# Kernel tuning notes

Hardware: AMD Instinct MI355X
Metric: run time of the kernel (lower is better)

## Reference

```python
import jax, jax.numpy as jnp
import numpy as np

DIM = 64; HEADS = 8; WIN = 4; K = 3
B = 8; H = 256; W = 256; WS = H // 2  # 2x2 window grid since ka_win_num=4
L = WIN * K * K            # 36 tokens for kernel self-attention
DH = DIM // HEADS
RED = DIM // 16            # SE reduction (dim>=64 branch)


def setup_inputs() -> dict:
    key = jax.random.key(0)
    ks = jax.random.split(key, 12)
    f = lambda k, s: jax.random.normal(k, s, jnp.float32) * 0.05
    return {
        "x": jax.random.normal(ks[0], (B, DIM, H, W), jnp.float32),
        "conv_w": f(ks[1], (WIN, DIM, DIM, K, K)),   # per-window Conv2d weights
        "w_qkv": f(ks[2], (3 * DIM, DIM)),
        "b_qkv": f(ks[3], (3 * DIM,)),
        "w_out": f(ks[4], (DIM, DIM)),
        "b_out": f(ks[5], (DIM,)),
        "se_w1": f(ks[6], (WIN, RED, DIM)),
        "se_b1": f(ks[7], (WIN, RED)),
        "se_w2": f(ks[8], (WIN, DIM, RED)),
        "se_b2": f(ks[9], (WIN, DIM)),
        "ln_w": jnp.ones((DIM,), jnp.float32),
        "ln_b": jnp.zeros((DIM,), jnp.float32),
    }


def reference(x, conv_w, w_qkv, b_qkv, w_out, b_out,
              se_w1, se_b1, se_w2, se_b2, ln_w, ln_b):
    Bx, C, Hx, Wx = x.shape
    ws = WS
    xw = x.reshape(Bx, C, 2, ws, 2, ws).transpose(2, 4, 0, 1, 3, 5)
    xw = xw.reshape(WIN, Bx, C, ws, ws)

    # ---- kernels from conv weights (conv output itself is discarded upstream)
    kern = conv_w.reshape(WIN, DIM, DIM, K * K).transpose(1, 0, 3, 2).reshape(DIM, L, DIM)

    # ---- tiny multi-head self-attention over the L kernel tokens, batch = DIM
    qkv = kern @ w_qkv.T + b_qkv                       # (DIM, L, 3*DIM)
    qkv = qkv.reshape(DIM, L, 3, HEADS, DH).transpose(2, 0, 3, 1, 4)  # (3, DIM, H, L, DH)
    q = qkv[0] * (DH ** -0.5)
    k_, v = qkv[1], qkv[2]
    attn = jax.nn.softmax(jnp.einsum('bhld,bhmd->bhlm', q, k_), axis=-1)
    out = jnp.einsum('bhlm,bhmd->bhld', attn, v)        # (DIM, H, L, DH)
    out = out.transpose(0, 2, 1, 3).reshape(DIM, L, DIM)
    kern = out @ w_out.T + b_out                        # (DIM, L, DIM)
    kern = kern.reshape(DIM, WIN, K, K, DIM).transpose(1, 0, 4, 2, 3)

    # ---- SE gating per window: pool over spatial, two 1x1 convs, sigmoid gate
    pooled = kern.mean(axis=(3, 4))
    h = jax.nn.relu(jnp.einsum('woi,wri->wor', pooled, se_w1) + se_b1[:, None, :])
    s = jax.nn.sigmoid(jnp.einsum('wor,wir->woi', h, se_w2) + se_b2[:, None, :])
    kern = kern * s[:, :, :, None, None]

    # ---- dynamic per-window conv2d (stride 1, pad 1)
    conv = lambda xi, wi: jax.lax.conv_general_dilated(
        xi, wi, window_strides=(1, 1), padding=((1, 1), (1, 1)))
    yw = jax.vmap(conv)(xw, kern)

    # ---- window reverse -> (B, C, H, W)
    y = yw.reshape(2, 2, Bx, C, ws, ws).transpose(2, 3, 0, 4, 1, 5).reshape(Bx, C, Hx, Wx)

    # ---- channel-last LayerNorm, then residual
    yt = y.transpose(0, 2, 3, 1)
    mu = yt.mean(-1, keepdims=True)
    var = yt.var(-1, keepdims=True)
    yt = (yt - mu) / jnp.sqrt(var + 1e-5) * ln_w + ln_b
    return x + yt.transpose(0, 3, 1, 2)
```

## Files before the change

kernel.cpp:

```cpp
#include <hip/hip_runtime.h>
#include <hip/hip_fp16.h>


typedef __attribute__((ext_vector_type(8))) _Float16 half8;
typedef __attribute__((ext_vector_type(4))) float floatx4;
typedef unsigned short ushort_t;

__device__ __forceinline__ ushort_t f2h(float f) {
  union { _Float16 h; ushort_t u; } cv;
  cv.h = (_Float16)f;
  return cv.u;
}

__device__ __align__(16) ushort_t g_W2[4 * 9 * 64 * 64];

__global__ __launch_bounds__(256) void tw_kernel(
    const float* __restrict__ conv_w,
    const float* __restrict__ w_qkv,
    const float* __restrict__ b_qkv,
    const float* __restrict__ w_out,
    const float* __restrict__ b_out,
    const float* __restrict__ se_w1,
    const float* __restrict__ se_b1,
    const float* __restrict__ se_w2,
    const float* __restrict__ se_b2)
{
  __shared__ __align__(16) float smem[11952];
  const int t = threadIdx.x;
  const int o = blockIdx.x;
  float* k0   = smem;
  float* qkvb = smem + 2448;
  float* aout = smem + 9504;

  for (int idx = t; idx < 36 * 64; idx += 256) {
    int l = idx >> 6, i = idx & 63;
    int win = l / 9, t9 = l - win * 9;
    k0[l * 68 + i] = conv_w[((win * 64 + o) * 64 + i) * 9 + t9];
  }
  __syncthreads();

  for (int idx = t; idx < 48 * 36; idx += 256) {
    int jg = idx / 36, l = idx - jg * 36;
    int j = jg << 2;
    const float* kr = k0 + l * 68;
    const float* w0 = w_qkv + j * 64;
    float a0 = 0.f, a1 = 0.f, a2 = 0.f, a3 = 0.f;
    #pragma unroll
    for (int i = 0; i < 64; i += 4) {
      floatx4 kf  = *(const floatx4*)(kr + i);
      floatx4 wf0 = *(const floatx4*)(w0 + i);
      floatx4 wf1 = *(const floatx4*)(w0 + 64 + i);
      floatx4 wf2 = *(const floatx4*)(w0 + 128 + i);
      floatx4 wf3 = *(const floatx4*)(w0 + 192 + i);
      #pragma unroll
      for (int e = 0; e < 4; ++e) {
        a0 += kf[e] * wf0[e];
        a1 += kf[e] * wf1[e];
        a2 += kf[e] * wf2[e];
        a3 += kf[e] * wf3[e];
      }
    }
    floatx4 r = { a0 + b_qkv[j],     a1 + b_qkv[j + 1],
                  a2 + b_qkv[j + 2], a3 + b_qkv[j + 3] };
    *(floatx4*)(qkvb + l * 196 + j) = r;
  }
  __syncthreads();

  for (int idx = t; idx < 288; idx += 256) {
    int h = idx / 36, l = idx - h * 36;
    const int hq = h << 3;
    floatx4 q0 = *(const floatx4*)(qkvb + l * 196 + hq);
    floatx4 q1 = *(const floatx4*)(qkvb + l * 196 + hq + 4);
    float sc[36];
    float mx = -1e30f;
    #pragma unroll
    for (int m = 0; m < 36; ++m) {
      const float* kr = qkvb + m * 196 + 64 + hq;
      floatx4 k0f = *(const floatx4*)(kr);
      floatx4 k1f = *(const floatx4*)(kr + 4);
      float s = 0.f;
      #pragma unroll
      for (int e = 0; e < 4; ++e) s += q0[e] * k0f[e];
      #pragma unroll
      for (int e = 0; e < 4; ++e) s += q1[e] * k1f[e];
      s *= 0.35355339059327373f;
      sc[m] = s;
      mx = fmaxf(mx, s);
    }
    float den = 0.f;
    #pragma unroll
    for (int m = 0; m < 36; ++m) { sc[m] = __expf(sc[m] - mx); den += sc[m]; }
    float a[8];
    #pragma unroll
    for (int e = 0; e < 8; ++e) a[e] = 0.f;
    #pragma unroll
    for (int m = 0; m < 36; ++m) {
      const float* vr = qkvb + m * 196 + 128 + hq;
      floatx4 v0f = *(const floatx4*)(vr);
      floatx4 v1f = *(const floatx4*)(vr + 4);
      float p = sc[m];
      #pragma unroll
      for (int e = 0; e < 4; ++e) { a[e] += p * v0f[e]; a[e + 4] += p * v1f[e]; }
    }
    float inv = 1.f / den;
    floatx4 o0, o1;
    #pragma unroll
    for (int e = 0; e < 4; ++e) { o0[e] = a[e] * inv; o1[e] = a[e + 4] * inv; }
    *(floatx4*)(aout + l * 68 + hq) = o0;
    *(floatx4*)(aout + l * 68 + hq + 4) = o1;
  }
  __syncthreads();

  float* mat = k0;
  for (int idx = t; idx < 16 * 36; idx += 256) {
    int og = idx / 36, l = idx - og * 36;
    int oo = og << 2;
    const float* ar = aout + l * 68;
    const float* w0 = w_out + oo * 64;
    float a0 = 0.f, a1 = 0.f, a2 = 0.f, a3 = 0.f;
    #pragma unroll
    for (int i = 0; i < 64; i += 4) {
      floatx4 af  = *(const floatx4*)(ar + i);
      floatx4 wf0 = *(const floatx4*)(w0 + i);
      floatx4 wf1 = *(const floatx4*)(w0 + 64 + i);
      floatx4 wf2 = *(const floatx4*)(w0 + 128 + i);
      floatx4 wf3 = *(const floatx4*)(w0 + 192 + i);
      #pragma unroll
      for (int e = 0; e < 4; ++e) {
        a0 += af[e] * wf0[e];
        a1 += af[e] * wf1[e];
        a2 += af[e] * wf2[e];
        a3 += af[e] * wf3[e];
      }
    }
    floatx4 r = { a0 + b_out[oo],     a1 + b_out[oo + 1],
                  a2 + b_out[oo + 2], a3 + b_out[oo + 3] };
    *(floatx4*)(mat + l * 68 + oo) = r;
  }
  __syncthreads();

  float* pl = qkvb;
  float* h1 = qkvb + 256;
  {
    int win = t >> 6, I = t & 63;
    float p = 0.f;
    #pragma unroll
    for (int t9 = 0; t9 < 9; ++t9) p += mat[(win * 9 + t9) * 68 + I];
    pl[t] = p * (1.f / 9.f);
  }
  __syncthreads();
  if (t < 16) {
    int win = t >> 2, r = t & 3;
    const float* wr = se_w1 + (win * 4 + r) * 64;
    const float* pr = pl + (win << 6);
    float a = se_b1[win * 4 + r];
    #pragma unroll 8
    for (int i = 0; i < 64; ++i) a += pr[i] * wr[i];
    h1[t] = fmaxf(a, 0.f);
  }
  __syncthreads();
  {
    int win = t >> 6, I = t & 63;
    float a = se_b2[(win << 6) + I];
    #pragma unroll
    for (int r = 0; r < 4; ++r)
      a += h1[win * 4 + r] * se_w2[((win << 6) + I) * 4 + r];
    float s = 1.f / (1.f + __expf(-a));
    #pragma unroll
    for (int t9 = 0; t9 < 9; ++t9) {
      float v = mat[(win * 9 + t9) * 68 + I] * s;
      g_W2[((win * 9 + t9) * 64 + o) * 64 + I] = f2h(v);
    }
  }
}

__global__ __launch_bounds__(256, 2) void conv_kernel(
    const float* __restrict__ x,
    const float* __restrict__ ln_w,
    const float* __restrict__ ln_b,
    float* __restrict__ outp)
{
  __shared__ __align__(16) short xs[24480];
  int* xs32 = (int*)xs;
  const int t = threadIdx.x;
  const int wsb = blockIdx.x & 1;
  const int hb  = (blockIdx.x >> 1) & 31;
  const int b   = blockIdx.x >> 6;
  const int gh0 = hb << 3;
  const int gws = wsb << 7;
  const int hlo = (gh0 >= 128) ? 128 : 0;
  const int wlo = gws;
  const int win = ((gh0 >= 128) ? 2 : 0) + wsb;
  const float* xb = x + ((size_t)b << 22);

  floatx4 sa0[5], sa1[5], sb0[5], sb1[5];
  float se0[3], se1[3];

  auto load_regs = [&](int gw0) {
    #pragma unroll
    for (int it = 0; it < 5; ++it) {
      int idx = t + it * 256;
      int u = idx & 3;
      int r = (idx >> 2) % 10;
      int cp = idx / 40;
      int gh = gh0 + r - 1;
      int gw = gw0 + (u << 3);
      floatx4 z = {0.f, 0.f, 0.f, 0.f};
      sa0[it] = z; sa1[it] = z; sb0[it] = z; sb1[it] = z;
      if (gh >= hlo && gh < hlo + 128) {
        const float* p = xb + ((size_t)(2 * cp) << 16) + gh * 256 + gw;
        sa0[it] = *(const floatx4*)p;
        sa1[it] = *(const floatx4*)(p + 4);
        sb0[it] = *(const floatx4*)(p + 65536);
        sb1[it] = *(const floatx4*)(p + 65540);
      }
    }
    #pragma unroll
    for (int it = 0; it < 3; ++it) {
      int idx = t + it * 256;
      se0[it] = 0.f; se1[it] = 0.f;
      if (idx < 640) {
        int e = idx & 1;
        int r = (idx >> 1) % 10;
        int cp = idx / 20;
        int gh = gh0 + r - 1;
        int gw = e ? (gw0 + 32) : (gw0 - 1);
        if (gh >= hlo && gh < hlo + 128 && gw >= wlo && gw < wlo + 128) {
          const float* p = xb + ((size_t)(2 * cp) << 16) + gh * 256 + gw;
          se0[it] = p[0];
          se1[it] = p[65536];
        }
      }
    }
  };

  auto write_lds = [&]() {
    #pragma unroll
    for (int it = 0; it < 5; ++it) {
      int idx = t + it * 256;
      int u = idx & 3;
      int r = (idx >> 2) % 10;
      int cp = idx / 40;
      int base = (r * 34 + (u << 3) + 1) * 36 + cp;
      #pragma unroll
      for (int j = 0; j < 4; ++j)
        xs32[base + j * 36] = (int)((unsigned)f2h(sa0[it][j]) |
                                    ((unsigned)f2h(sb0[it][j]) << 16));
      #pragma unroll
      for (int j = 0; j < 4; ++j)
        xs32[base + (j + 4) * 36] = (int)((unsigned)f2h(sa1[it][j]) |
                                          ((unsigned)f2h(sb1[it][j]) << 16));
    }
    #pragma unroll
    for (int it = 0; it < 3; ++it) {
      int idx = t + it * 256;
      if (idx < 640) {
        int e = idx & 1;
        int r = (idx >> 1) % 10;
        int cp = idx / 20;
        int cl = e ? 33 : 0;
        xs32[(r * 34 + cl) * 36 + cp] = (int)((unsigned)f2h(se0[it]) |
                                              ((unsigned)f2h(se1[it]) << 16));
      }
    }
  };

  const int wave = t >> 6, lane = t & 63;
  const int l15 = lane & 15, q = lane >> 4;

  int aoff[4];
  #pragma unroll
  for (int mt = 0; mt < 4; ++mt)
    aoff[mt] = ((2 * wave + (mt >> 1)) * 34 + ((mt & 1) << 4) + l15) * 72 + (q << 3);

  const ushort_t* Wb = g_W2 + win * 36864 + l15 * 64 + (q << 3);

  float lnwv[4], lnbv[4];
  #pragma unroll
  for (int nt = 0; nt < 4; ++nt) {
    int c = (nt << 4) + l15;
    lnwv[nt] = ln_w[c];
    lnbv[nt] = ln_b[c];
  }

  load_regs(gws);
  write_lds();
  __syncthreads();

  #pragma unroll 1
  for (int c = 0; c < 4; ++c) {
    const int gw0 = gws + (c << 5);
    if (c < 3) load_regs(gws + ((c + 1) << 5));

    floatx4 acc[4][4];
    #pragma unroll
    for (int mt = 0; mt < 4; ++mt)
      #pragma unroll
      for (int nt = 0; nt < 4; ++nt)
        acc[mt][nt] = (floatx4){0.f, 0.f, 0.f, 0.f};

    half8 bcur[4], bnxt[4];
    #pragma unroll
    for (int nt = 0; nt < 4; ++nt)
      bcur[nt] = *(const half8*)(Wb + nt * 1024);

    #pragma unroll
    for (int tap = 0; tap < 9; ++tap) {
      const int ky = tap / 3, kx = tap - ky * 3;
      const int toff = (ky * 34 + kx) * 72;
      #pragma unroll
      for (int kc = 0; kc < 2; ++kc) {
        const int nit = tap * 2 + kc + 1;
        if (nit < 18) {
          const int ntap = nit >> 1, nkc = nit & 1;
          #pragma unroll
          for (int nt = 0; nt < 4; ++nt)
            bnxt[nt] = *(const half8*)(Wb + ntap * 4096 + nkc * 32 + nt * 1024);
        }
        half8 av[4];
        #pragma unroll
        for (int mt = 0; mt < 4; ++mt)
          av[mt] = *(const half8*)(xs + aoff[mt] + toff + kc * 32);
        #pragma unroll
        for (int mt = 0; mt < 4; ++mt)
          #pragma unroll
          for (int nt = 0; nt < 4; ++nt)
            acc[mt][nt] = __builtin_amdgcn_mfma_f32_16x16x32_f16(
                av[mt], bcur[nt], acc[mt][nt], 0, 0, 0);
        #pragma unroll
        for (int nt = 0; nt < 4; ++nt) bcur[nt] = bnxt[nt];
      }
    }

    #pragma unroll
    for (int mt = 0; mt < 4; ++mt) {
      const int rr = 2 * wave + (mt >> 1);
      const int colb = (mt & 1) << 4;
      floatx4 xr[4];
      size_t goffs[4];
      #pragma unroll
      for (int nt = 0; nt < 4; ++nt) {
        const int ch = (nt << 4) + l15;
        goffs[nt] = ((size_t)(b * 64 + ch) << 16) +
                    (gh0 + rr) * 256 + gw0 + colb + (q << 2);
        xr[nt] = *(const floatx4*)(x + goffs[nt]);
      }
      float s1[4], s2[4];
      #pragma unroll
      for (int e = 0; e < 4; ++e) { s1[e] = 0.f; s2[e] = 0.f; }
      #pragma unroll
      for (int nt = 0; nt < 4; ++nt)
        #pragma unroll
        for (int e = 0; e < 4; ++e) {
          float v = acc[mt][nt][e];
          s1[e] += v;
          s2[e] += v * v;
        }
      #pragma unroll
      for (int m = 1; m < 16; m <<= 1) {
        #pragma unroll
        for (int e = 0; e < 4; ++e) {
          s1[e] += __shfl_xor(s1[e], m, 64);
          s2[e] += __shfl_xor(s2[e], m, 64);
        }
      }
      float mean[4], rstd[4];
      #pragma unroll
      for (int e = 0; e < 4; ++e) {
        mean[e] = s1[e] * 0.015625f;
        float var = s2[e] * 0.015625f - mean[e] * mean[e];
        rstd[e] = rsqrtf(var + 1e-5f);
      }
      #pragma unroll
      for (int nt = 0; nt < 4; ++nt) {
        floatx4 v;
        #pragma unroll
        for (int e = 0; e < 4; ++e)
          v[e] = (acc[mt][nt][e] - mean[e]) * rstd[e] * lnwv[nt] + lnbv[nt] + xr[nt][e];
        *(floatx4*)(outp + goffs[nt]) = v;
      }
    }

    if (c < 3) {
      __syncthreads();
      write_lds();
      __syncthreads();
    }
  }
}

extern "C" void kernel_launch(void* const* d_in, const int* in_sizes, int n_in,
                              void* d_out, int out_size, void* d_ws, size_t ws_size,
                              hipStream_t stream) {
  const float* x     = (const float*)d_in[0];
  const float* convw = (const float*)d_in[1];
  const float* wqkv  = (const float*)d_in[2];
  const float* bqkv  = (const float*)d_in[3];
  const float* wout  = (const float*)d_in[4];
  const float* bout  = (const float*)d_in[5];
  const float* sew1  = (const float*)d_in[6];
  const float* seb1  = (const float*)d_in[7];
  const float* sew2  = (const float*)d_in[8];
  const float* seb2  = (const float*)d_in[9];
  const float* lnw   = (const float*)d_in[10];
  const float* lnb   = (const float*)d_in[11];
  float* outp = (float*)d_out;

  hipLaunchKernelGGL(tw_kernel, dim3(64), dim3(256), 0, stream,
                     convw, wqkv, bqkv, wout, bout,
                     sew1, seb1, sew2, seb2);
  hipLaunchKernelGGL(conv_kernel, dim3(512), dim3(256), 0, stream,
                     x, lnw, lnb, outp);
}
```

Measured before the change: 495.8 us.

## Split conv blocks into single 32-column tiles and read residual from LDS

Result: faster. 402.8 us (-18.8%).

```diff
diff --git a/kernel.cpp b/kernel.cpp
--- a/kernel.cpp
+++ b/kernel.cpp
@@ -174,7 +174,7 @@
   }
 }
 
-__global__ __launch_bounds__(256, 2) void conv_kernel(
+__global__ __launch_bounds__(256, 3) void conv_kernel(
     const float* __restrict__ x,
     const float* __restrict__ ln_w,
     const float* __restrict__ ln_b,
@@ -183,98 +183,134 @@
   __shared__ __align__(16) short xs[24480];
   int* xs32 = (int*)xs;
   const int t = threadIdx.x;
-  const int wsb = blockIdx.x & 1;
-  const int hb  = (blockIdx.x >> 1) & 31;
-  const int b   = blockIdx.x >> 6;
-  const int gh0 = hb << 3;
-  const int gws = wsb << 7;
+  const int wb = blockIdx.x & 7;
+  const int hb = (blockIdx.x >> 3) & 31;
+  const int b  = blockIdx.x >> 8;
+  const int gh0 = hb << 3, gw0 = wb << 5;
   const int hlo = (gh0 >= 128) ? 128 : 0;
-  const int wlo = gws;
-  const int win = ((gh0 >= 128) ? 2 : 0) + wsb;
+  const int wlo = (gw0 >= 128) ? 128 : 0;
+  const int win = ((gh0 >= 128) ? 2 : 0) + ((gw0 >= 128) ? 1 : 0);
   const float* xb = x + ((size_t)b << 22);
 
   floatx4 sa0[5], sa1[5], sb0[5], sb1[5];
   float se0[3], se1[3];
-
-  auto load_regs = [&](int gw0) {
-    #pragma unroll
-    for (int it = 0; it < 5; ++it) {
-      int idx = t + it * 256;
-      int u = idx & 3;
-      int r = (idx >> 2) % 10;
-      int cp = idx / 40;
+  #pragma unroll
+  for (int it = 0; it < 5; ++it) {
+    int idx = t + it * 256;
+    int u = idx & 3;
+    int r = (idx >> 2) % 10;
+    int cp = idx / 40;
+    int gh = gh0 + r - 1;
+    int gw = gw0 + (u << 3);
+    floatx4 z = {0.f, 0.f, 0.f, 0.f};
+    sa0[it] = z; sa1[it] = z; sb0[it] = z; sb1[it] = z;
+    if (gh >= hlo && gh < hlo + 128) {
+      const float* p = xb + ((size_t)(2 * cp) << 16) + gh * 256 + gw;
+      sa0[it] = *(const floatx4*)p;
+      sa1[it] = *(const floatx4*)(p + 4);
+      sb0[it] = *(const floatx4*)(p + 65536);
+      sb1[it] = *(const floatx4*)(p + 65540);
+    }
+  }
+  #pragma unroll
+  for (int it = 0; it < 3; ++it) {
+    int idx = t + it * 256;
+    se0[it] = 0.f; se1[it] = 0.f;
+    if (idx < 640) {
+      int e = idx & 1;
+      int r = (idx >> 1) % 10;
+      int cp = idx / 20;
       int gh = gh0 + r - 1;
-      int gw = gw0 + (u << 3);
-      floatx4 z = {0.f, 0.f, 0.f, 0.f};
-      sa0[it] = z; sa1[it] = z; sb0[it] = z; sb1[it] = z;
-      if (gh >= hlo && gh < hlo + 128) {
+      int gw = e ? (gw0 + 32) : (gw0 - 1);
+      if (gh >= hlo && gh < hlo + 128 && gw >= wlo && gw < wlo + 128) {
         const float* p = xb + ((size_t)(2 * cp) << 16) + gh * 256 + gw;
-        sa0[it] = *(const floatx4*)p;
-        sa1[it] = *(const floatx4*)(p + 4);
-        sb0[it] = *(const floatx4*)(p + 65536);
-        sb1[it] = *(const floatx4*)(p + 65540);
-      }
-    }
-    #pragma unroll
-    for (int it = 0; it < 3; ++it) {
-      int idx = t + it * 256;
-      se0[it] = 0.f; se1[it] = 0.f;
-      if (idx < 640) {
-        int e = idx & 1;
-        int r = (idx >> 1) % 10;
-        int cp = idx / 20;
-        int gh = gh0 + r - 1;
-        int gw = e ? (gw0 + 32) : (gw0 - 1);
-        if (gh >= hlo && gh < hlo + 128 && gw >= wlo && gw < wlo + 128) {
-          const float* p = xb + ((size_t)(2 * cp) << 16) + gh * 256 + gw;
-          se0[it] = p[0];
-          se1[it] = p[65536];
-        }
-      }
-    }
-  };
-
-  auto write_lds = [&]() {
-    #pragma unroll
-    for (int it = 0; it < 5; ++it) {
-      int idx = t + it * 256;
-      int u = idx & 3;
-      int r = (idx >> 2) % 10;
-      int cp = idx / 40;
-      int base = (r * 34 + (u << 3) + 1) * 36 + cp;
-      #pragma unroll
-      for (int j = 0; j < 4; ++j)
-        xs32[base + j * 36] = (int)((unsigned)f2h(sa0[it][j]) |
-                                    ((unsigned)f2h(sb0[it][j]) << 16));
-      #pragma unroll
-      for (int j = 0; j < 4; ++j)
-        xs32[base + (j + 4) * 36] = (int)((unsigned)f2h(sa1[it][j]) |
-                                          ((unsigned)f2h(sb1[it][j]) << 16));
-    }
-    #pragma unroll
-    for (int it = 0; it < 3; ++it) {
-      int idx = t + it * 256;
-      if (idx < 640) {
-        int e = idx & 1;
-        int r = (idx >> 1) % 10;
-        int cp = idx / 20;
-        int cl = e ? 33 : 0;
-        xs32[(r * 34 + cl) * 36 + cp] = (int)((unsigned)f2h(se0[it]) |
-                                              ((unsigned)f2h(se1[it]) << 16));
-      }
-    }
-  };
+        se0[it] = p[0];
+        se1[it] = p[65536];
+      }
+    }
+  }
+  __builtin_amdgcn_sched_barrier(0);
+
+  #pragma unroll
+  for (int it = 0; it < 5; ++it) {
+    int idx = t + it * 256;
+    int u = idx & 3;
+    int r = (idx >> 2) % 10;
+    int cp = idx / 40;
+    int base = (r * 34 + (u << 3) + 1) * 36 + cp;
+    #pragma unroll
+    for (int j = 0; j < 4; ++j)
+      xs32[base + j * 36] = (int)((unsigned)f2h(sa0[it][j]) |
+                                  ((unsigned)f2h(sb0[it][j]) << 16));
+    #pragma unroll
+    for (int j = 0; j < 4; ++j)
+      xs32[base + (j + 4) * 36] = (int)((unsigned)f2h(sa1[it][j]) |
+                                        ((unsigned)f2h(sb1[it][j]) << 16));
+  }
+  #pragma unroll
+  for (int it = 0; it < 3; ++it) {
+    int idx = t + it * 256;
+    if (idx < 640) {
+      int e = idx & 1;
+      int r = (idx >> 1) % 10;
+      int cp = idx / 20;
+      int cl = e ? 33 : 0;
+      xs32[(r * 34 + cl) * 36 + cp] = (int)((unsigned)f2h(se0[it]) |
+                                            ((unsigned)f2h(se1[it]) << 16));
+    }
+  }
+  __syncthreads();
 
   const int wave = t >> 6, lane = t & 63;
   const int l15 = lane & 15, q = lane >> 4;
 
+  floatx4 acc[4][4];
+  #pragma unroll
+  for (int mt = 0; mt < 4; ++mt)
+    #pragma unroll
+    for (int nt = 0; nt < 4; ++nt)
+      acc[mt][nt] = (floatx4){0.f, 0.f, 0.f, 0.f};
+
   int aoff[4];
   #pragma unroll
   for (int mt = 0; mt < 4; ++mt)
     aoff[mt] = ((2 * wave + (mt >> 1)) * 34 + ((mt & 1) << 4) + l15) * 72 + (q << 3);
 
   const ushort_t* Wb = g_W2 + win * 36864 + l15 * 64 + (q << 3);
-
+  half8 bcur[4], bnxt[4];
+  #pragma unroll
+  for (int nt = 0; nt < 4; ++nt)
+    bcur[nt] = *(const half8*)(Wb + nt * 1024);
+
+  #pragma unroll
+  for (int tap = 0; tap < 9; ++tap) {
+    const int ky = tap / 3, kx = tap - ky * 3;
+    const int toff = (ky * 34 + kx) * 72;
+    #pragma unroll
+    for (int kc = 0; kc < 2; ++kc) {
+      const int nit = tap * 2 + kc + 1;
+      if (nit < 18) {
+        const int ntap = nit >> 1, nkc = nit & 1;
+        #pragma unroll
+        for (int nt = 0; nt < 4; ++nt)
+          bnxt[nt] = *(const half8*)(Wb + ntap * 4096 + nkc * 32 + nt * 1024);
+      }
+      half8 av[4];
+      #pragma unroll
+      for (int mt = 0; mt < 4; ++mt)
+        av[mt] = *(const half8*)(xs + aoff[mt] + toff + kc * 32);
+      #pragma unroll
+      for (int mt = 0; mt < 4; ++mt)
+        #pragma unroll
+        for (int nt = 0; nt < 4; ++nt)
+          acc[mt][nt] = __builtin_amdgcn_mfma_f32_16x16x32_f16(
+              av[mt], bcur[nt], acc[mt][nt], 0, 0, 0);
+      #pragma unroll
+      for (int nt = 0; nt < 4; ++nt) bcur[nt] = bnxt[nt];
+    }
+  }
+
+  const _Float16* xh = (const _Float16*)xs;
   float lnwv[4], lnbv[4];
   #pragma unroll
   for (int nt = 0; nt < 4; ++nt) {
@@ -282,109 +318,56 @@
     lnwv[nt] = ln_w[c];
     lnbv[nt] = ln_b[c];
   }
-
-  load_regs(gws);
-  write_lds();
-  __syncthreads();
-
-  #pragma unroll 1
-  for (int c = 0; c < 4; ++c) {
-    const int gw0 = gws + (c << 5);
-    if (c < 3) load_regs(gws + ((c + 1) << 5));
-
-    floatx4 acc[4][4];
-    #pragma unroll
-    for (int mt = 0; mt < 4; ++mt)
-      #pragma unroll
-      for (int nt = 0; nt < 4; ++nt)
-        acc[mt][nt] = (floatx4){0.f, 0.f, 0.f, 0.f};
-
-    half8 bcur[4], bnxt[4];
+  #pragma unroll
+  for (int mt = 0; mt < 4; ++mt) {
+    const int rr = 2 * wave + (mt >> 1);
+    const int colb = (mt & 1) << 4;
+    const int pxb = ((rr + 1) * 34 + 1 + colb + (q << 2)) * 72;
+    float xr[4][4];
+    #pragma unroll
+    for (int s = 0; s < 4; ++s) {
+      const int nt = (s + q) & 3;
+      const int ch = (nt << 4) + l15;
+      #pragma unroll
+      for (int e = 0; e < 4; ++e)
+        xr[nt][e] = (float)xh[pxb + e * 72 + ch];
+    }
+    float s1[4], s2[4];
+    #pragma unroll
+    for (int e = 0; e < 4; ++e) { s1[e] = 0.f; s2[e] = 0.f; }
     #pragma unroll
     for (int nt = 0; nt < 4; ++nt)
-      bcur[nt] = *(const half8*)(Wb + nt * 1024);
-
-    #pragma unroll
-    for (int tap = 0; tap < 9; ++tap) {
-      const int ky = tap / 3, kx = tap - ky * 3;
-      const int toff = (ky * 34 + kx) * 72;
-      #pragma unroll
-      for (int kc = 0; kc < 2; ++kc) {
-        const int nit = tap * 2 + kc + 1;
-        if (nit < 18) {
-          const int ntap = nit >> 1, nkc = nit & 1;
-          #pragma unroll
-          for (int nt = 0; nt < 4; ++nt)
-            bnxt[nt] = *(const half8*)(Wb + ntap * 4096 + nkc * 32 + nt * 1024);
-        }
-        half8 av[4];
-        #pragma unroll
-        for (int mt = 0; mt < 4; ++mt)
-          av[mt] = *(const half8*)(xs + aoff[mt] + toff + kc * 32);
-        #pragma unroll
-        for (int mt = 0; mt < 4; ++mt)
-          #pragma unroll
-          for (int nt = 0; nt < 4; ++nt)
-            acc[mt][nt] = __builtin_amdgcn_mfma_f32_16x16x32_f16(
-                av[mt], bcur[nt], acc[mt][nt], 0, 0, 0);
-        #pragma unroll
-        for (int nt = 0; nt < 4; ++nt) bcur[nt] = bnxt[nt];
-      }
-    }
-
-    #pragma unroll
-    for (int mt = 0; mt < 4; ++mt) {
-      const int rr = 2 * wave + (mt >> 1);
-      const int colb = (mt & 1) << 4;
-      floatx4 xr[4];
-      size_t goffs[4];
-      #pragma unroll
-      for (int nt = 0; nt < 4; ++nt) {
-        const int ch = (nt << 4) + l15;
-        goffs[nt] = ((size_t)(b * 64 + ch) << 16) +
-                    (gh0 + rr) * 256 + gw0 + colb + (q << 2);
-        xr[nt] = *(const floatx4*)(x + goffs[nt]);
-      }
-      float s1[4], s2[4];
-      #pragma unroll
-      for (int e = 0; e < 4; ++e) { s1[e] = 0.f; s2[e] = 0.f; }
-      #pragma unroll
-      for (int nt = 0; nt < 4; ++nt)
-        #pragma unroll
-        for (int e = 0; e < 4; ++e) {
-          float v = acc[mt][nt][e];
-          s1[e] += v;
-          s2[e] += v * v;
-        }
-      #pragma unroll
-      for (int m = 1; m < 16; m <<= 1) {
-        #pragma unroll
-        for (int e = 0; e < 4; ++e) {
-          s1[e] += __shfl_xor(s1[e], m, 64);
-          s2[e] += __shfl_xor(s2[e], m, 64);
-        }
-      }
-      float mean[4], rstd[4];
       #pragma unroll
       for (int e = 0; e < 4; ++e) {
-        mean[e] = s1[e] * 0.015625f;
-        float var = s2[e] * 0.015625f - mean[e] * mean[e];
-        rstd[e] = rsqrtf(var + 1e-5f);
-      }
-      #pragma unroll
-      for (int nt = 0; nt < 4; ++nt) {
-        floatx4 v;
-        #pragma unroll
-        for (int e = 0; e < 4; ++e)
-          v[e] = (acc[mt][nt][e] - mean[e]) * rstd[e] * lnwv[nt] + lnbv[nt] + xr[nt][e];
-        *(floatx4*)(outp + goffs[nt]) = v;
-      }
-    }
-
-    if (c < 3) {
-      __syncthreads();
-      write_lds();
-      __syncthreads();
+        float v = acc[mt][nt][e];
+        s1[e] += v;
+        s2[e] += v * v;
+      }
+    #pragma unroll
+    for (int m = 1; m < 16; m <<= 1) {
+      #pragma unroll
+      for (int e = 0; e < 4; ++e) {
+        s1[e] += __shfl_xor(s1[e], m, 64);
+        s2[e] += __shfl_xor(s2[e], m, 64);
+      }
+    }
+    float mean[4], rstd[4];
+    #pragma unroll
+    for (int e = 0; e < 4; ++e) {
+      mean[e] = s1[e] * 0.015625f;
+      float var = s2[e] * 0.015625f - mean[e] * mean[e];
+      rstd[e] = rsqrtf(var + 1e-5f);
+    }
+    #pragma unroll
+    for (int nt = 0; nt < 4; ++nt) {
+      const int c = (nt << 4) + l15;
+      const size_t goff = ((size_t)(b * 64 + c) << 16) +
+                          (gh0 + rr) * 256 + gw0 + colb + (q << 2);
+      floatx4 v;
+      #pragma unroll
+      for (int e = 0; e < 4; ++e)
+        v[e] = (acc[mt][nt][e] - mean[e]) * rstd[e] * lnwv[nt] + lnbv[nt] + xr[nt][e];
+      *(floatx4*)(outp + goff) = v;
     }
   }
 }
@@ -409,6 +392,6 @@
   hipLaunchKernelGGL(tw_kernel, dim3(64), dim3(256), 0, stream,
                      convw, wqkv, bqkv, wout, bout,
                      sew1, seb1, sew2, seb2);
-  hipLaunchKernelGGL(conv_kernel, dim3(512), dim3(256), 0, stream,
+  hipLaunchKernelGGL(conv_kernel, dim3(2048), dim3(256), 0, stream,
                      x, lnw, lnb, outp);
 }
```
